# Optimization experiments

Hardware: AMD Instinct MI355X
Metric: run time of the kernel (lower is better)

The kernel has to match this reference:

```python
import jax, jax.numpy as jnp
import numpy as np

EPSILON = 0.05
SINKHORN_ITERS = 3
TEMP = 0.1
PROB_RATIO = 1.0
LAMBD = 15.0
MU = 1.0
NU = 1.0
GAMMA = 0.2

B, D, K = 16384, 512, 2048


def setup_inputs() -> dict:
    key = jax.random.key(0)
    k1, k2, k3 = jax.random.split(key, 3)
    z_1 = jax.random.normal(k1, (B, D), dtype=jnp.float32)
    z_2 = jax.random.normal(k2, (B, D), dtype=jnp.float32)
    W = jax.random.normal(k3, (K, D), dtype=jnp.float32) * (1.0 / np.sqrt(D))
    return {"z_1": z_1, "z_2": z_2, "W": W}


def _compute_v(z):
    # unbiased variance over batch dim, matching torch.var default
    var = jnp.var(z, axis=0, ddof=1)
    return jnp.mean(jnp.maximum(0.0, GAMMA - jnp.sqrt(var + 1e-8)))


def _compute_c(z):
    n, d = z.shape
    zc = z - jnp.mean(z, axis=0, keepdims=True)
    C = (zc.T @ zc) / (n - 1)  # [d, d] unbiased covariance (torch.cov)
    off = C - jnp.diag(jnp.diag(C))
    return jnp.sum(off * off) / d


def _l2norm(z):
    return z / jnp.clip(jnp.linalg.norm(z, axis=-1, keepdims=True), 1e-12)


def _sinkhorn(out):
    # out: [B, K] raw logits (no grad path)
    b, k = out.shape
    Q = jnp.exp(out / EPSILON).T  # [K, B]
    Q = Q / jnp.sum(Q)
    for _ in range(SINKHORN_ITERS):
        Q = Q / (jnp.sum(Q, axis=1, keepdims=True) * k)
        Q = Q / (jnp.sum(Q, axis=0, keepdims=True) * b)
    Q = Q * b
    return Q.T  # [B, K]


def reference(z_1, z_2, W):
    v_z1 = _compute_v(z_1)
    v_z2 = _compute_v(z_2)
    c_z1 = _compute_c(z_1)
    c_z2 = _compute_c(z_2)

    z1n = _l2norm(z_1)
    z2n = _l2norm(z_2)
    logits_1 = z1n @ W.T  # [B, K]
    logits_2 = z2n @ W.T

    tgt_w_1 = jax.lax.stop_gradient(logits_1 * PROB_RATIO + logits_2 * (1 - PROB_RATIO))
    tgt_w_2 = jax.lax.stop_gradient(logits_2 * PROB_RATIO + logits_1 * (1 - PROB_RATIO))
    tgt_probs_1 = _sinkhorn(tgt_w_1)
    tgt_probs_2 = _sinkhorn(tgt_w_2)

    l1 = logits_1 / TEMP
    l2 = logits_2 / TEMP
    lp1 = jax.nn.log_softmax(l1, axis=1)
    lp2 = jax.nn.log_softmax(l2, axis=1)

    loss_ce = -0.5 * (jnp.mean(jnp.sum(tgt_probs_1 * lp2, axis=1))
                      + jnp.mean(jnp.sum(tgt_probs_2 * lp1, axis=1)))
    loss_var = v_z1 + v_z2
    loss_cov = c_z1 + c_z2
    loss = LAMBD * loss_ce + MU * loss_var + NU * loss_cov

    # diagnostics (no-grad in original)
    logits = jnp.concatenate([l1, l2], axis=0)  # [2B, K]
    k_idx = jnp.argmax(logits, axis=-1)
    hard_probs = jnp.zeros((K,), logits.dtype).at[k_idx].add(1.0) / logits.shape[0]
    code_perplexity = jnp.exp(-jnp.sum(hard_probs * jnp.log(hard_probs + 1e-7)))
    avg_probs = jnp.mean(jax.nn.softmax(logits, axis=-1), axis=0)
    prob_perplexity = jnp.exp(-jnp.sum(avg_probs * jnp.log(avg_probs + 1e-7)))
    acc_1 = jnp.mean((jnp.argmax(l1, axis=1) == jnp.argmax(tgt_probs_2, axis=1)).astype(jnp.float32))
    acc_2 = jnp.mean((jnp.argmax(l2, axis=1) == jnp.argmax(tgt_probs_1, axis=1)).astype(jnp.float32))
    acc = 0.5 * (acc_1 + acc_2)

    return (loss, loss_ce, loss_var, loss_cov, code_perplexity, prob_perplexity, acc)
```

## Files before the change

kernel.cpp:

```cpp
#include <hip/hip_runtime.h>
#include <hip/hip_bf16.h>

#define B_N 16384
#define D_N 512
#define K_N 2048

typedef __attribute__((ext_vector_type(8))) short bf16x8;
typedef __attribute__((ext_vector_type(4))) float f32x4;
typedef __attribute__((ext_vector_type(4))) unsigned short u16x4;
typedef unsigned short u16;

__device__ __forceinline__ float bf2f(short s) {
  return __builtin_bit_cast(float, ((unsigned)(u16)s) << 16);
}
__device__ __forceinline__ u16 f2bf(float x) {
  return __builtin_bit_cast(u16, __float2bfloat16(x));
}
__device__ __forceinline__ unsigned fbits(float x) {
  return __builtin_bit_cast(unsigned, x);
}
__device__ __forceinline__ float wred_sum(float v) {
#pragma unroll
  for (int o = 32; o; o >>= 1) v += __shfl_down(v, o, 64);
  return v;
}

__device__ __forceinline__ void gld16(const u16* g, const u16* l) {
  __builtin_amdgcn_global_load_lds((const __attribute__((address_space(1))) void*)g,
                                   (__attribute__((address_space(3))) void*)l, 16, 0, 0);
}

__global__ __launch_bounds__(256) void k_rownorm(const float* __restrict__ z1,
                                                 const float* __restrict__ z2,
                                                 u16* __restrict__ zn1, u16* __restrict__ zn2,
                                                 u16* __restrict__ zb1, u16* __restrict__ zb2) {
  int wid = threadIdx.x >> 6, lane = threadIdx.x & 63;
  int row = blockIdx.x * 4 + wid;
  const float* z; u16 *zn, *zb; int r;
  if (row < B_N) { z = z1; zn = zn1; zb = zb1; r = row; }
  else { z = z2; zn = zn2; zb = zb2; r = row - B_N; }
  const float4* zr = (const float4*)(z + (size_t)r * D_N);
  float4 va = zr[lane], vb = zr[lane + 64];
  float ss = va.x*va.x + va.y*va.y + va.z*va.z + va.w*va.w
           + vb.x*vb.x + vb.y*vb.y + vb.z*vb.z + vb.w*vb.w;
#pragma unroll
  for (int o = 32; o; o >>= 1) ss += __shfl_xor(ss, o, 64);
  float inv = 1.0f / fmaxf(sqrtf(ss), 1e-12f);
  u16x4 pa = {f2bf(va.x), f2bf(va.y), f2bf(va.z), f2bf(va.w)};
  u16x4 pb = {f2bf(vb.x), f2bf(vb.y), f2bf(vb.z), f2bf(vb.w)};
  u16x4 na = {f2bf(va.x*inv), f2bf(va.y*inv), f2bf(va.z*inv), f2bf(va.w*inv)};
  u16x4 nb = {f2bf(vb.x*inv), f2bf(vb.y*inv), f2bf(vb.z*inv), f2bf(vb.w*inv)};
  ((u16x4*)(zb + (size_t)r * D_N))[lane] = pa;
  ((u16x4*)(zb + (size_t)r * D_N))[lane + 64] = pb;
  ((u16x4*)(zn + (size_t)r * D_N))[lane] = na;
  ((u16x4*)(zn + (size_t)r * D_N))[lane + 64] = nb;
}

__global__ __launch_bounds__(256) void k_convW(const float* __restrict__ W,
                                               u16* __restrict__ Wb) {
  size_t base = ((size_t)blockIdx.x * 256 + threadIdx.x) * 8;
#pragma unroll
  for (int j = 0; j < 8; j++) Wb[base + j] = f2bf(W[base + j]);
}

__global__ __launch_bounds__(512) void k_colstats(const u16* __restrict__ zb1,
                                                  const u16* __restrict__ zb2,
                                                  float* __restrict__ csum,
                                                  float* __restrict__ csumsq) {
  int zi = blockIdx.z;
  const u16* z = zi ? zb2 : zb1;
  __shared__ float s1[512], s2[512];
  int t = threadIdx.y * 64 + threadIdx.x;
  s1[t] = 0.f; s2[t] = 0.f;
  __syncthreads();
  int c0 = threadIdx.x * 8;
  float a[8], a2[8];
#pragma unroll
  for (int e = 0; e < 8; e++) { a[e] = 0.f; a2[e] = 0.f; }
  for (int u = 0; u < 16; u++) {
    int r = blockIdx.y * 128 + threadIdx.y + 8 * u;
    bf16x8 v = *(const bf16x8*)&z[(size_t)r * D_N + c0];
#pragma unroll
    for (int e = 0; e < 8; e++) { float x = bf2f(v[e]); a[e] += x; a2[e] += x * x; }
  }
#pragma unroll
  for (int e = 0; e < 8; e++) {
    atomicAdd(&s1[c0 + e], a[e]);
    atomicAdd(&s2[c0 + e], a2[e]);
  }
  __syncthreads();
  atomicAdd(&csum[zi * D_N + t], s1[t]);
  atomicAdd(&csumsq[zi * D_N + t], s2[t]);
}

__global__ __launch_bounds__(256) void k_vloss(const float* __restrict__ csum,
                                               const float* __restrict__ csumsq,
                                               float* __restrict__ scal) {
  int idx = blockIdx.x * 256 + threadIdx.x;
  float s = csum[idx], sq = csumsq[idx];
  float mean = s * (1.0f / (float)B_N);
  float var = (sq - (float)B_N * mean * mean) * (1.0f / (float)(B_N - 1));
  float term = fmaxf(0.f, 0.2f - sqrtf(var + 1e-8f));
  term = wred_sum(term);
  __shared__ float sw[4];
  if ((threadIdx.x & 63) == 0) sw[threadIdx.x >> 6] = term;
  __syncthreads();
  if (threadIdx.x == 0) atomicAdd(&scal[0], sw[0] + sw[1] + sw[2] + sw[3]);
}

__global__ __launch_bounds__(256) void k_gram(const u16* __restrict__ zb1,
                                              const u16* __restrict__ zb2,
                                              float* __restrict__ Gpart) {
  int zi = blockIdx.z >> 4, chunk = blockIdx.z & 15;
  const u16* z = zi ? zb2 : zb1;
  int ti = 0, xx = blockIdx.x;
  while (xx >= 8 - ti) { xx -= 8 - ti; ti++; }
  int tj = ti + xx;
  int i0 = ti * 64, j0 = tj * 64;
  __shared__ u16 lA[64][32], lB[64][32];
  int t = threadIdx.x, wid = t >> 6, lane = t & 63;
  int br = t & 31, fg = t >> 5;
  f32x4 acc[4];
#pragma unroll
  for (int q = 0; q < 4; q++) acc[q] = (f32x4){0.f, 0.f, 0.f, 0.f};
  for (int bb = 0; bb < 1024; bb += 32) {
    size_t rb = ((size_t)chunk * 1024 + bb + br) * D_N;
    bf16x8 va = *(const bf16x8*)&z[rb + i0 + fg * 8];
    bf16x8 vb = *(const bf16x8*)&z[rb + j0 + fg * 8];
#pragma unroll
    for (int e = 0; e < 8; e++) {
      lA[fg * 8 + e][br] = (u16)va[e];
      lB[fg * 8 + e][br] = (u16)vb[e];
    }
    __syncthreads();
    int m = lane & 15, q = lane >> 4;
    bf16x8 a = *(const bf16x8*)&lA[16 * wid + m][8 * q];
#pragma unroll
    for (int tt = 0; tt < 4; tt++) {
      bf16x8 b = *(const bf16x8*)&lB[16 * tt + m][8 * q];
      acc[tt] = __builtin_amdgcn_mfma_f32_16x16x32_bf16(a, b, acc[tt], 0, 0, 0);
    }
    __syncthreads();
  }
  float* gp = Gpart + (((size_t)zi * 16 + chunk) * 36 + blockIdx.x) * 4096;
  int n = lane & 15, q = lane >> 4;
#pragma unroll
  for (int tt = 0; tt < 4; tt++)
#pragma unroll
    for (int r = 0; r < 4; r++)
      gp[(16 * wid + q * 4 + r) * 64 + 16 * tt + n] = acc[tt][r];
}

__global__ __launch_bounds__(256) void k_covreduce(const float* __restrict__ Gpart,
                                                   const float* __restrict__ csum,
                                                   float* __restrict__ scal) {
  int zi = blockIdx.y;
  int tile = blockIdx.x >> 4, part = blockIdx.x & 15;
  int ti = 0, xx = tile;
  while (xx >= 8 - ti) { xx -= 8 - ti; ti++; }
  int tj = ti + xx;
  int idx = part * 256 + threadIdx.x;
  int li = idx >> 6, lj = idx & 63;
  int i = ti * 64 + li, j = tj * 64 + lj;
  float g = 0.f;
#pragma unroll
  for (int c = 0; c < 16; c++)
    g += Gpart[(((size_t)zi * 16 + c) * 36 + tile) * 4096 + idx];
  float mi = csum[zi * D_N + i] * (1.0f / (float)B_N);
  float mj = csum[zi * D_N + j] * (1.0f / (float)B_N);
  float C = (g - (float)B_N * mi * mj) * (1.0f / (float)(B_N - 1));
  float wgt = (ti == tj) ? ((li == lj) ? 0.f : 1.f) : 2.f;
  float v = wgt * C * C;
  v = wred_sum(v);
  __shared__ float sw[4];
  if ((threadIdx.x & 63) == 0) sw[threadIdx.x >> 6] = v;
  __syncthreads();
  if (threadIdx.x == 0) atomicAdd(&scal[1], sw[0] + sw[1] + sw[2] + sw[3]);
}

__global__ __launch_bounds__(256) void k_logits(const u16* __restrict__ zn1,
                                                const u16* __restrict__ zn2,
                                                const u16* __restrict__ Wb,
                                                u16* __restrict__ L1, u16* __restrict__ L2,
                                                float* __restrict__ rowsum) {
  int zi = blockIdx.z;
  const u16* A = zi ? zn2 : zn1;
  u16* Lout = zi ? L2 : L1;
  int b0 = blockIdx.x * 128, k0 = blockIdx.y * 128;
  __shared__ u16 lA[128 * 64], lB[128 * 64];
  int t = threadIdx.x, lane = t & 63, wid = t >> 6;
  int wm = wid >> 1, wn = wid & 1;
  f32x4 acc[4][4];
#pragma unroll
  for (int i = 0; i < 4; i++)
#pragma unroll
    for (int j = 0; j < 4; j++) acc[i][j] = (f32x4){0.f, 0.f, 0.f, 0.f};
  int srow = t >> 3;
  int sseg = t & 7;
  int ldsoff = (t & 192) * 16;
  for (int d0 = 0; d0 < D_N; d0 += 64) {
#pragma unroll
    for (int qo = 0; qo < 4; qo++) {
      int row = qo * 32 + srow;
      int scol = (sseg ^ (row & 7)) * 8;
      gld16(A + (size_t)(b0 + row) * D_N + d0 + scol,
            (const u16*)((const char*)lA + qo * 4096 + ldsoff));
      gld16(Wb + (size_t)(k0 + row) * D_N + d0 + scol,
            (const u16*)((const char*)lB + qo * 4096 + ldsoff));
    }
    __syncthreads();
#pragma unroll
    for (int ks = 0; ks < 2; ks++) {
      bf16x8 af[4], bfr[4];
#pragma unroll
      for (int i = 0; i < 4; i++) {
        int row = wm * 64 + i * 16 + (lane & 15);
        int seg = (ks * 4 + (lane >> 4)) ^ (row & 7);
        af[i] = *(const bf16x8*)((const char*)lA + row * 128 + seg * 16);
      }
#pragma unroll
      for (int j = 0; j < 4; j++) {
        int row = wn * 64 + j * 16 + (lane & 15);
        int seg = (ks * 4 + (lane >> 4)) ^ (row & 7);
        bfr[j] = *(const bf16x8*)((const char*)lB + row * 128 + seg * 16);
      }
#pragma unroll
      for (int i = 0; i < 4; i++)
#pragma unroll
        for (int j = 0; j < 4; j++)
          acc[i][j] = __builtin_amdgcn_mfma_f32_16x16x32_bf16(bfr[j], af[i], acc[i][j], 0, 0, 0);
    }
    __syncthreads();
  }
  float* red = (float*)lA;
  if (t < 128) red[t] = 0.f;
  __syncthreads();
  int cb = lane & 15;
  int cq = lane >> 4;
  float rp[16];
#pragma unroll
  for (int q = 0; q < 16; q++) rp[q] = 0.f;
#pragma unroll
  for (int i = 0; i < 4; i++)
#pragma unroll
    for (int j = 0; j < 4; j++) {
      f32x4 v = acc[i][j];
      u16x4 h = {f2bf(v[0]), f2bf(v[1]), f2bf(v[2]), f2bf(v[3])};
      int gb = b0 + wm * 64 + i * 16 + cb;
      int gk = k0 + wn * 64 + j * 16 + cq * 4;
      *(u16x4*)&Lout[(size_t)gb * K_N + gk] = h;
#pragma unroll
      for (int r = 0; r < 4; r++)
        rp[j * 4 + r] += __expf(20.0f * bf2f((short)h[r]));
    }
#pragma unroll
  for (int q = 0; q < 16; q++) {
#pragma unroll
    for (int o = 1; o < 16; o <<= 1) rp[q] += __shfl_xor(rp[q], o, 64);
  }
  if (cb == 0) {
#pragma unroll
    for (int j = 0; j < 4; j++)
#pragma unroll
      for (int r = 0; r < 4; r++)
        atomicAdd(&red[wn * 64 + j * 16 + cq * 4 + r], rp[j * 4 + r]);
  }
  __syncthreads();
  if (t < 128) atomicAdd(&rowsum[(size_t)zi * 3 * K_N + k0 + t], red[t]);
}

__global__ __launch_bounds__(256) void k_sink(const u16* __restrict__ L1,
                                              const u16* __restrict__ L2,
                                              float* __restrict__ rowsum, int it) {
  int zi = blockIdx.y;
  const u16* L = zi ? L2 : L1;
  const float* rs_in = rowsum + ((size_t)zi * 3 + it) * K_N;
  float* rs_out = rowsum + ((size_t)zi * 3 + it + 1) * K_N;
  __shared__ float pm[K_N];
  int t = threadIdx.x, lane = t & 63, wid = t >> 6;
  for (int k = t; k < K_N; k += 256) pm[k] = 0.f;
  float rv[32];
#pragma unroll
  for (int jj = 0; jj < 4; jj++) {
    const float4* p = (const float4*)&rs_in[jj * 512 + lane * 8];
    float4 x = p[0], y = p[1];
    rv[jj*8+0] = 1.0f / ((float)K_N * x.x); rv[jj*8+1] = 1.0f / ((float)K_N * x.y);
    rv[jj*8+2] = 1.0f / ((float)K_N * x.z); rv[jj*8+3] = 1.0f / ((float)K_N * x.w);
    rv[jj*8+4] = 1.0f / ((float)K_N * y.x); rv[jj*8+5] = 1.0f / ((float)K_N * y.y);
    rv[jj*8+6] = 1.0f / ((float)K_N * y.z); rv[jj*8+7] = 1.0f / ((float)K_N * y.w);
  }
  __syncthreads();
  float racc[32];
#pragma unroll
  for (int q = 0; q < 32; q++) racc[q] = 0.f;
  int w = blockIdx.x * 4 + wid;
  for (int rr = 0; rr < 8; rr++) {
    int b = w * 8 + rr;
    float ex[32];
    float c = 0.f;
#pragma unroll
    for (int jj = 0; jj < 4; jj++) {
      bf16x8 v = *(const bf16x8*)&L[(size_t)b * K_N + jj * 512 + lane * 8];
#pragma unroll
      for (int e = 0; e < 8; e++) {
        float E = __expf(20.0f * bf2f(v[e]));
        ex[jj * 8 + e] = E;
        c += E * rv[jj * 8 + e];
      }
    }
#pragma unroll
    for (int o = 32; o; o >>= 1) c += __shfl_xor(c, o, 64);
    float cb = 1.0f / ((float)B_N * c);
#pragma unroll
    for (int q = 0; q < 32; q++) racc[q] += ex[q] * cb;
  }
#pragma unroll
  for (int q = 0; q < 32; q++)
    atomicAdd(&pm[(q & 7) * 256 + (q >> 3) * 64 + lane], racc[q]);
  __syncthreads();
  for (int k = t; k < K_N; k += 256)
    atomicAdd(&rs_out[k], pm[(k & 7) * 256 + (k >> 3)]);
}

__global__ __launch_bounds__(256, 2) void k_final(const u16* __restrict__ L1,
                                                  const u16* __restrict__ L2,
                                                  const float* __restrict__ rowsum,
                                                  float* __restrict__ probsum,
                                                  int* __restrict__ counts,
                                                  float* __restrict__ scal) {
  __shared__ float pmerge[K_N];
  const float* rs1 = rowsum + 2 * K_N;
  const float* rs2 = rowsum + 5 * K_N;
  int t = threadIdx.x, lane = t & 63, wid = t >> 6;
  for (int k = t; k < K_N; k += 256) pmerge[k] = 0.f;
  float rv1[32], rv2[32];
#pragma unroll
  for (int jj = 0; jj < 4; jj++) {
    const float4* p1 = (const float4*)&rs1[jj * 512 + lane * 8];
    const float4* p2 = (const float4*)&rs2[jj * 512 + lane * 8];
    float4 x1 = p1[0], y1 = p1[1], x2 = p2[0], y2 = p2[1];
    rv1[jj*8+0] = 1.0f/((float)K_N*x1.x); rv1[jj*8+1] = 1.0f/((float)K_N*x1.y);
    rv1[jj*8+2] = 1.0f/((float)K_N*x1.z); rv1[jj*8+3] = 1.0f/((float)K_N*x1.w);
    rv1[jj*8+4] = 1.0f/((float)K_N*y1.x); rv1[jj*8+5] = 1.0f/((float)K_N*y1.y);
    rv1[jj*8+6] = 1.0f/((float)K_N*y1.z); rv1[jj*8+7] = 1.0f/((float)K_N*y1.w);
    rv2[jj*8+0] = 1.0f/((float)K_N*x2.x); rv2[jj*8+1] = 1.0f/((float)K_N*x2.y);
    rv2[jj*8+2] = 1.0f/((float)K_N*x2.z); rv2[jj*8+3] = 1.0f/((float)K_N*x2.w);
    rv2[jj*8+4] = 1.0f/((float)K_N*y2.x); rv2[jj*8+5] = 1.0f/((float)K_N*y2.y);
    rv2[jj*8+6] = 1.0f/((float)K_N*y2.z); rv2[jj*8+7] = 1.0f/((float)K_N*y2.w);
  }
  __syncthreads();
  float pacc[32];
#pragma unroll
  for (int q = 0; q < 32; q++) pacc[q] = 0.f;
  float ce_acc = 0.f; int acc_cnt = 0;
  int w = blockIdx.x * 4 + wid;
  for (int pp = 0; pp < 8; pp++) {
    int ba = w * 16 + pp * 2;
    bf16x8 va1[4], va2[4], vb1[4], vb2[4];
#pragma unroll
    for (int jj = 0; jj < 4; jj++) {
      va1[jj] = *(const bf16x8*)&L1[(size_t)ba * K_N + jj * 512 + lane * 8];
      va2[jj] = *(const bf16x8*)&L2[(size_t)ba * K_N + jj * 512 + lane * 8];
      vb1[jj] = *(const bf16x8*)&L1[(size_t)(ba + 1) * K_N + jj * 512 + lane * 8];
      vb2[jj] = *(const bf16x8*)&L2[(size_t)(ba + 1) * K_N + jj * 512 + lane * 8];
    }
    float sE1a=0,sE2a=0,d12a=0,d21a=0,Z1a=0,Z2a=0;
    float sE1b=0,sE2b=0,d12b=0,d21b=0,Z1b=0,Z2b=0;
    unsigned um1a=0,um2a=0,ua1a=0,ua2a=0;
    unsigned um1b=0,um2b=0,ua1b=0,ua2b=0;
#pragma unroll
    for (int jj = 0; jj < 4; jj++)
#pragma unroll
      for (int e = 0; e < 8; e++) {
        int q = jj * 8 + e;
        unsigned ik = 2047u - (unsigned)(jj * 512 + lane * 8 + e);
        float x1 = bf2f(va1[jj][e]), x2 = bf2f(va2[jj][e]);
        float t1 = __expf(10.0f * x1), t2 = __expf(10.0f * x2);
        float e1 = t1 * t1 * rv1[q], e2 = t2 * t2 * rv2[q];
        sE1a += e1; sE2a += e2; d12a += e1 * x2; d21a += e2 * x1; Z1a += t1; Z2a += t2;
        um1a = max(um1a, (fbits(t1) & 0xFFFFF800u) | ik);
        um2a = max(um2a, (fbits(t2) & 0xFFFFF800u) | ik);
        ua1a = max(ua1a, (fbits(e1) & 0xFFFFF800u) | ik);
        ua2a = max(ua2a, (fbits(e2) & 0xFFFFF800u) | ik);
        x1 = bf2f(vb1[jj][e]); x2 = bf2f(vb2[jj][e]);
        t1 = __expf(10.0f * x1); t2 = __expf(10.0f * x2);
        e1 = t1 * t1 * rv1[q]; e2 = t2 * t2 * rv2[q];
        sE1b += e1; sE2b += e2; d12b += e1 * x2; d21b += e2 * x1; Z1b += t1; Z2b += t2;
        um1b = max(um1b, (fbits(t1) & 0xFFFFF800u) | ik);
        um2b = max(um2b, (fbits(t2) & 0xFFFFF800u) | ik);
        ua1b = max(ua1b, (fbits(e1) & 0xFFFFF800u) | ik);
        ua2b = max(ua2b, (fbits(e2) & 0xFFFFF800u) | ik);
      }
#pragma unroll
    for (int o = 32; o; o >>= 1) {
      sE1a += __shfl_xor(sE1a, o, 64); sE2a += __shfl_xor(sE2a, o, 64);
      d12a += __shfl_xor(d12a, o, 64); d21a += __shfl_xor(d21a, o, 64);
      Z1a += __shfl_xor(Z1a, o, 64);   Z2a += __shfl_xor(Z2a, o, 64);
      sE1b += __shfl_xor(sE1b, o, 64); sE2b += __shfl_xor(sE2b, o, 64);
      d12b += __shfl_xor(d12b, o, 64); d21b += __shfl_xor(d21b, o, 64);
      Z1b += __shfl_xor(Z1b, o, 64);   Z2b += __shfl_xor(Z2b, o, 64);
      um1a = max(um1a, (unsigned)__shfl_xor((int)um1a, o, 64));
      um2a = max(um2a, (unsigned)__shfl_xor((int)um2a, o, 64));
      ua1a = max(ua1a, (unsigned)__shfl_xor((int)ua1a, o, 64));
      ua2a = max(ua2a, (unsigned)__shfl_xor((int)ua2a, o, 64));
      um1b = max(um1b, (unsigned)__shfl_xor((int)um1b, o, 64));
      um2b = max(um2b, (unsigned)__shfl_xor((int)um2b, o, 64));
      ua1b = max(ua1b, (unsigned)__shfl_xor((int)ua1b, o, 64));
      ua2b = max(ua2b, (unsigned)__shfl_xor((int)ua2b, o, 64));
    }
    {
      int m1i = 2047 - (int)(um1a & 2047u), m2i = 2047 - (int)(um2a & 2047u);
      int a1i = 2047 - (int)(ua1a & 2047u), a2i = 2047 - (int)(ua2a & 2047u);
      float invc1 = 1.0f / sE1a, invc2 = 1.0f / sE2a;
      ce_acc += (10.0f * d12a) * invc1 - __logf(Z2a) + (10.0f * d21a) * invc2 - __logf(Z1a);
      acc_cnt += (m1i == a2i) + (m2i == a1i);
      if (lane == 0) { atomicAdd(&counts[m1i], 1); atomicAdd(&counts[m2i], 1); }
      float iZ1 = 1.0f / Z1a, iZ2 = 1.0f / Z2a;
#pragma unroll
      for (int jj = 0; jj < 4; jj++)
#pragma unroll
        for (int e = 0; e < 8; e++)
          pacc[jj * 8 + e] += __expf(10.0f * bf2f(va1[jj][e])) * iZ1
                            + __expf(10.0f * bf2f(va2[jj][e])) * iZ2;
    }
    {
      int m1i = 2047 - (int)(um1b & 2047u), m2i = 2047 - (int)(um2b & 2047u);
      int a1i = 2047 - (int)(ua1b & 2047u), a2i = 2047 - (int)(ua2b & 2047u);
      float invc1 = 1.0f / sE1b, invc2 = 1.0f / sE2b;
      ce_acc += (10.0f * d12b) * invc1 - __logf(Z2b) + (10.0f * d21b) * invc2 - __logf(Z1b);
      acc_cnt += (m1i == a2i) + (m2i == a1i);
      if (lane == 0) { atomicAdd(&counts[m1i], 1); atomicAdd(&counts[m2i], 1); }
      float iZ1 = 1.0f / Z1b, iZ2 = 1.0f / Z2b;
#pragma unroll
      for (int jj = 0; jj < 4; jj++)
#pragma unroll
        for (int e = 0; e < 8; e++)
          pacc[jj * 8 + e] += __expf(10.0f * bf2f(vb1[jj][e])) * iZ1
                            + __expf(10.0f * bf2f(vb2[jj][e])) * iZ2;
    }
  }
  if (lane == 0) {
    atomicAdd(&scal[2], ce_acc);
    atomicAdd(&scal[3], (float)acc_cnt);
  }
#pragma unroll
  for (int q = 0; q < 32; q++)
    atomicAdd(&pmerge[(q & 7) * 256 + (q >> 3) * 64 + lane], pacc[q]);
  __syncthreads();
  for (int k = t; k < K_N; k += 256) atomicAdd(&probsum[k], pmerge[k]);
}

__global__ __launch_bounds__(256) void k_combine(const float* __restrict__ scal,
                                                 const float* __restrict__ probsum,
                                                 const int* __restrict__ counts,
                                                 float* __restrict__ out) {
  int t = threadIdx.x;
  float ec = 0.f, ep = 0.f;
  for (int k = t; k < K_N; k += 256) {
    float p = (float)counts[k] * (1.0f / (2.0f * (float)B_N));
    ec += -p * __logf(p + 1e-7f);
    float q = probsum[k] * (1.0f / (2.0f * (float)B_N));
    ep += -q * __logf(q + 1e-7f);
  }
  ec = wred_sum(ec);
  ep = wred_sum(ep);
  __shared__ float se[4], sp[4];
  if ((t & 63) == 0) { se[t >> 6] = ec; sp[t >> 6] = ep; }
  __syncthreads();
  if (t == 0) {
    float tec = se[0] + se[1] + se[2] + se[3];
    float tep = sp[0] + sp[1] + sp[2] + sp[3];
    float ce = -0.5f * scal[2] * (1.0f / (float)B_N);
    float lvar = scal[0] * (1.0f / (float)D_N);
    float lcov = scal[1] * (1.0f / (float)D_N);
    float acc = scal[3] * (1.0f / (2.0f * (float)B_N));
    out[0] = 15.0f * ce + lvar + lcov;
    out[1] = ce;
    out[2] = lvar;
    out[3] = lcov;
    out[4] = __expf(tec);
    out[5] = __expf(tep);
    out[6] = acc;
  }
}

extern "C" void kernel_launch(void* const* d_in, const int* in_sizes, int n_in,
                              void* d_out, int out_size, void* d_ws, size_t ws_size,
                              hipStream_t stream) {
  (void)in_sizes; (void)n_in; (void)out_size; (void)ws_size;
  const float* z1 = (const float*)d_in[0];
  const float* z2 = (const float*)d_in[1];
  const float* W = (const float*)d_in[2];

  char* w = (char*)d_ws;
  size_t off = 0;
  auto take = [&](size_t b) -> void* {
    void* p = w + off;
    off = (off + b + 255) & ~(size_t)255;
    return p;
  };
  float* rowsum = (float*)take(2 * 3 * K_N * 4);
  float* csum = (float*)take(2 * D_N * 4);
  float* csumsq = (float*)take(2 * D_N * 4);
  float* probsum = (float*)take(K_N * 4);
  int* counts = (int*)take(K_N * 4);
  float* scal = (float*)take(64);
  size_t zero_bytes = off;
  u16* zn1 = (u16*)take((size_t)B_N * D_N * 2);
  u16* zn2 = (u16*)take((size_t)B_N * D_N * 2);
  u16* Wb = (u16*)take((size_t)K_N * D_N * 2);
  u16* L1 = (u16*)take((size_t)B_N * K_N * 2);
  u16* L2 = (u16*)take((size_t)B_N * K_N * 2);
  float* Gpart = (float*)take((size_t)2 * 16 * 36 * 4096 * 4);
  u16* zb1 = L1;
  u16* zb2 = L1 + (size_t)B_N * D_N;

  hipMemsetAsync(d_ws, 0, zero_bytes, stream);

  k_rownorm<<<8192, 256, 0, stream>>>(z1, z2, zn1, zn2, zb1, zb2);
  k_convW<<<512, 256, 0, stream>>>(W, Wb);
  k_colstats<<<dim3(1, 128, 2), dim3(64, 8), 0, stream>>>(zb1, zb2, csum, csumsq);
  k_vloss<<<4, 256, 0, stream>>>(csum, csumsq, scal);
  k_gram<<<dim3(36, 1, 32), 256, 0, stream>>>(zb1, zb2, Gpart);
  k_covreduce<<<dim3(36 * 16, 2), 256, 0, stream>>>(Gpart, csum, scal);
  k_logits<<<dim3(128, 16, 2), 256, 0, stream>>>(zn1, zn2, Wb, L1, L2, rowsum);
  k_sink<<<dim3(512, 2), 256, 0, stream>>>(L1, L2, rowsum, 0);
  k_sink<<<dim3(512, 2), 256, 0, stream>>>(L1, L2, rowsum, 1);
  k_final<<<256, 256, 0, stream>>>(L1, L2, rowsum, probsum, counts, scal);
  k_combine<<<1, 256, 0, stream>>>(scal, probsum, counts, (float*)d_out);
}
```

Baseline: 552.3 us.

## Restructure logits GEMM to 256x256 tiles with double-buffered LDS pipeline

The logits GEMM moves from 128x128 tiles with 256 threads to 256x256 tiles with 512 threads. LDS is double-buffered (128 KB) so loads for the next K slice overlap MFMA work, using explicit waitcnt and barriers. It also adds MFMA priority hints and a remapped block order meant to improve L2 reuse. The aim is more data reuse per tile and hidden global-load latency, at the cost of higher register pressure and fewer blocks (1024) to fill the CUs.

```diff
diff --git a/kernel.cpp b/kernel.cpp
--- a/kernel.cpp
+++ b/kernel.cpp
@@ -178,62 +178,95 @@
   if (threadIdx.x == 0) atomicAdd(&scal[1], sw[0] + sw[1] + sw[2] + sw[3]);
 }
 
-__global__ __launch_bounds__(256) void k_logits(const u16* __restrict__ zn1,
-                                                const u16* __restrict__ zn2,
-                                                const u16* __restrict__ Wb,
-                                                u16* __restrict__ L1, u16* __restrict__ L2,
-                                                float* __restrict__ rowsum) {
-  int zi = blockIdx.z;
+__device__ __forceinline__ bf16x8 fragld(const u16* base, int row, int ks, int lane) {
+  int seg = (ks * 4 + (lane >> 4)) ^ (row & 7);
+  return *(const bf16x8*)&base[row * 64 + seg * 8];
+}
+
+__device__ __forceinline__ void stage256(const u16* __restrict__ G, int grow0,
+                                         int d0, const u16* ldsbase, int t) {
+#pragma unroll
+  for (int q = 0; q < 4; q++) {
+    int row = q * 64 + (t >> 3);
+    int scol = ((t & 7) ^ ((t >> 3) & 7)) * 8;
+    gld16(G + (size_t)(grow0 + row) * D_N + d0 + scol,
+          ldsbase + q * 4096 + (t >> 6) * 512);
+  }
+}
+
+__device__ __forceinline__ void comp256(const u16* tA, const u16* tB,
+                                        f32x4 (&acc)[8][4], int wm, int wn, int lane) {
+  bf16x8 bq[4][2];
+#pragma unroll
+  for (int j = 0; j < 4; j++)
+#pragma unroll
+    for (int ks = 0; ks < 2; ks++)
+      bq[j][ks] = fragld(tB, wn * 64 + j * 16 + (lane & 15), ks, lane);
+#pragma unroll
+  for (int q = 0; q < 4; q++) {
+    bf16x8 aq[2][2];
+#pragma unroll
+    for (int i2 = 0; i2 < 2; i2++)
+#pragma unroll
+      for (int ks = 0; ks < 2; ks++)
+        aq[i2][ks] = fragld(tA, wm * 128 + (q * 2 + i2) * 16 + (lane & 15), ks, lane);
+    __builtin_amdgcn_s_setprio(1);
+#pragma unroll
+    for (int i2 = 0; i2 < 2; i2++)
+#pragma unroll
+      for (int j = 0; j < 4; j++)
+#pragma unroll
+        for (int ks = 0; ks < 2; ks++)
+          acc[q * 2 + i2][j] = __builtin_amdgcn_mfma_f32_16x16x32_bf16(
+              bq[j][ks], aq[i2][ks], acc[q * 2 + i2][j], 0, 0, 0);
+    __builtin_amdgcn_s_setprio(0);
+  }
+}
+
+__global__ __launch_bounds__(512, 2) void k_logits(const u16* __restrict__ zn1,
+                                                   const u16* __restrict__ zn2,
+                                                   const u16* __restrict__ Wb,
+                                                   u16* __restrict__ L1, u16* __restrict__ L2,
+                                                   float* __restrict__ rowsum) {
+  __shared__ u16 lds[65536];
+  int hw = blockIdx.x + 64 * (blockIdx.y + 8 * blockIdx.z);
+  int l = (hw & 7) * 128 + (hw >> 3);
+  int zi = l >> 9, by = (l >> 6) & 7, bx = l & 63;
   const u16* A = zi ? zn2 : zn1;
   u16* Lout = zi ? L2 : L1;
-  int b0 = blockIdx.x * 128, k0 = blockIdx.y * 128;
-  __shared__ u16 lA[128 * 64], lB[128 * 64];
+  int b0 = bx * 256, k0 = by * 256;
   int t = threadIdx.x, lane = t & 63, wid = t >> 6;
-  int wm = wid >> 1, wn = wid & 1;
-  f32x4 acc[4][4];
-#pragma unroll
-  for (int i = 0; i < 4; i++)
+  int wm = wid >> 2, wn = wid & 3;
+  f32x4 acc[8][4];
+#pragma unroll
+  for (int i = 0; i < 8; i++)
 #pragma unroll
     for (int j = 0; j < 4; j++) acc[i][j] = (f32x4){0.f, 0.f, 0.f, 0.f};
-  int srow = t >> 3;
-  int sseg = t & 7;
-  int ldsoff = (t & 192) * 16;
-  for (int d0 = 0; d0 < D_N; d0 += 64) {
-#pragma unroll
-    for (int qo = 0; qo < 4; qo++) {
-      int row = qo * 32 + srow;
-      int scol = (sseg ^ (row & 7)) * 8;
-      gld16(A + (size_t)(b0 + row) * D_N + d0 + scol,
-            (const u16*)((const char*)lA + qo * 4096 + ldsoff));
-      gld16(Wb + (size_t)(k0 + row) * D_N + d0 + scol,
-            (const u16*)((const char*)lB + qo * 4096 + ldsoff));
-    }
-    __syncthreads();
-#pragma unroll
-    for (int ks = 0; ks < 2; ks++) {
-      bf16x8 af[4], bfr[4];
-#pragma unroll
-      for (int i = 0; i < 4; i++) {
-        int row = wm * 64 + i * 16 + (lane & 15);
-        int seg = (ks * 4 + (lane >> 4)) ^ (row & 7);
-        af[i] = *(const bf16x8*)((const char*)lA + row * 128 + seg * 16);
-      }
-#pragma unroll
-      for (int j = 0; j < 4; j++) {
-        int row = wn * 64 + j * 16 + (lane & 15);
-        int seg = (ks * 4 + (lane >> 4)) ^ (row & 7);
-        bfr[j] = *(const bf16x8*)((const char*)lB + row * 128 + seg * 16);
-      }
-#pragma unroll
-      for (int i = 0; i < 4; i++)
-#pragma unroll
-        for (int j = 0; j < 4; j++)
-          acc[i][j] = __builtin_amdgcn_mfma_f32_16x16x32_bf16(bfr[j], af[i], acc[i][j], 0, 0, 0);
-    }
-    __syncthreads();
-  }
-  float* red = (float*)lA;
-  if (t < 128) red[t] = 0.f;
+
+  stage256(A, b0, 0, lds, t);
+  stage256(Wb, k0, 0, lds + 16384, t);
+  stage256(A, b0, 64, lds + 32768, t);
+  stage256(Wb, k0, 64, lds + 49152, t);
+  asm volatile("s_waitcnt vmcnt(8)\n\ts_barrier" ::: "memory");
+
+#pragma unroll
+  for (int kt = 0; kt < 8; kt++) {
+    const u16* tA = lds + (kt & 1) * 32768;
+    comp256(tA, tA + 16384, acc, wm, wn, lane);
+    if (kt < 6) {
+      asm volatile("s_barrier" ::: "memory");
+      const u16* dst = lds + (kt & 1) * 32768;
+      stage256(A, b0, (kt + 2) * 64, dst, t);
+      stage256(Wb, k0, (kt + 2) * 64, dst + 16384, t);
+      asm volatile("s_waitcnt vmcnt(8)\n\ts_barrier" ::: "memory");
+    } else if (kt == 6) {
+      asm volatile("s_waitcnt vmcnt(0)\n\ts_barrier" ::: "memory");
+    }
+  }
+
+  __syncthreads();
+  float* red = (float*)lds;
+  if (t < 256) red[t] = 0.f;
   __syncthreads();
   int cb = lane & 15;
   int cq = lane >> 4;
@@ -241,12 +274,12 @@
 #pragma unroll
   for (int q = 0; q < 16; q++) rp[q] = 0.f;
 #pragma unroll
-  for (int i = 0; i < 4; i++)
+  for (int i = 0; i < 8; i++)
 #pragma unroll
     for (int j = 0; j < 4; j++) {
       f32x4 v = acc[i][j];
       u16x4 h = {f2bf(v[0]), f2bf(v[1]), f2bf(v[2]), f2bf(v[3])};
-      int gb = b0 + wm * 64 + i * 16 + cb;
+      int gb = b0 + wm * 128 + i * 16 + cb;
       int gk = k0 + wn * 64 + j * 16 + cq * 4;
       *(u16x4*)&Lout[(size_t)gb * K_N + gk] = h;
 #pragma unroll
@@ -266,7 +299,7 @@
         atomicAdd(&red[wn * 64 + j * 16 + cq * 4 + r], rp[j * 4 + r]);
   }
   __syncthreads();
-  if (t < 128) atomicAdd(&rowsum[(size_t)zi * 3 * K_N + k0 + t], red[t]);
+  if (t < 256) atomicAdd(&rowsum[(size_t)zi * 3 * K_N + k0 + t], red[t]);
 }
 
 __global__ __launch_bounds__(256) void k_sink(const u16* __restrict__ L1,
@@ -523,7 +556,7 @@
   k_vloss<<<4, 256, 0, stream>>>(csum, csumsq, scal);
   k_gram<<<dim3(36, 1, 32), 256, 0, stream>>>(zb1, zb2, Gpart);
   k_covreduce<<<dim3(36 * 16, 2), 256, 0, stream>>>(Gpart, csum, scal);
-  k_logits<<<dim3(128, 16, 2), 256, 0, stream>>>(zn1, zn2, Wb, L1, L2, rowsum);
+  k_logits<<<dim3(64, 8, 2), 512, 0, stream>>>(zn1, zn2, Wb, L1, L2, rowsum);
   k_sink<<<dim3(512, 2), 256, 0, stream>>>(L1, L2, rowsum, 0);
   k_sink<<<dim3(512, 2), 256, 0, stream>>>(L1, L2, rowsum, 1);
   k_final<<<256, 256, 0, stream>>>(L1, L2, rowsum, probsum, counts, scal);
```

Result: faster. 537.1 us (-2.8%).
